# Kernel optimization log

Measured on AMD Instinct MI355X. Metric: run time of the kernel, lower is better.

The kernel has to match this reference:

```python
import jax, jax.numpy as jnp
import numpy as np

B, S, L, D = 32, 8, 128, 768
A, T = 10, 8
VOCAB = 1000


def setup_inputs() -> dict:
    key = jax.random.key(0)
    k1, k2, k3, k4, k5 = jax.random.split(key, 5)
    sentence_ids = jax.random.randint(k1, (B, S, L), 0, VOCAB)
    sentence_attention_masks = jnp.ones((B, S, L), dtype=jnp.float32)
    # precomputed sum of last 4 BERT hidden layers (backbone excluded)
    sentence_embeddings = jax.random.normal(k2, (B, S, L, D), dtype=jnp.float32)
    predicate_ids = jax.random.randint(k3, (B, S, A, T), 0, VOCAB)
    arg0_ids = jax.random.randint(k4, (B, S, A, T), 0, VOCAB)
    arg1_ids = jax.random.randint(k5, (B, S, A, T), 0, VOCAB)
    return {
        "sentence_ids": sentence_ids,
        "sentence_attention_masks": sentence_attention_masks,
        "sentence_embeddings": sentence_embeddings,
        "predicate_ids": predicate_ids,
        "arg0_ids": arg0_ids,
        "arg1_ids": arg1_ids,
    }


def _mean_pool(emb, mask):
    # emb: [b,s,l,d], mask: [b,s,l] -> [b,s,d]
    masked_sum = jnp.einsum('bsld,bsl->bsd', emb, mask)
    counts = jnp.clip(mask.sum(-1, keepdims=True), 1, None)
    return masked_sum / counts


def _arg_embedding(arg_ids, sentence_ids, emb):
    # arg_ids: [b,s,a,t] int, sentence_ids: [b,s,l] int, emb: [b,s,l,d]
    # match[b,s,a,t,l] = sentence token l equals arg token t (and arg token != 0)
    match = (sentence_ids[:, :, None, None, :] == arg_ids[..., None]) & (arg_ids[..., None] != 0)
    mf = match.astype(emb.dtype)
    counts = mf.sum(-1)                                   # [b,s,a,t]
    summed = jnp.einsum('bsatl,bsld->bsatd', mf, emb)      # [b,s,a,t,d]
    avg = summed / jnp.maximum(counts, 1.0)[..., None]
    has = counts > 0                                       # [b,s,a,t]
    t_dim = arg_ids.shape[-1]
    # original loop overwrites per token -> keep the LAST token with a match
    last = (t_dim - 1) - jnp.argmax(has[..., ::-1], axis=-1)  # [b,s,a]
    sel = jnp.take_along_axis(avg, last[..., None, None], axis=3)[:, :, :, 0, :]
    valid = has.any(-1)                                    # [b,s,a]
    return jnp.where(valid[..., None], sel, jnp.zeros((), emb.dtype))


def reference(sentence_ids, sentence_attention_masks, sentence_embeddings,
              predicate_ids, arg0_ids, arg1_ids):
    sentence_embeddings_avg = _mean_pool(sentence_embeddings, sentence_attention_masks)
    predicate_embeddings = _arg_embedding(predicate_ids, sentence_ids, sentence_embeddings)
    arg0_embeddings = _arg_embedding(arg0_ids, sentence_ids, sentence_embeddings)
    arg1_embeddings = _arg_embedding(arg1_ids, sentence_ids, sentence_embeddings)
    return (sentence_embeddings_avg, predicate_embeddings, arg0_embeddings, arg1_embeddings)
```

## Files before the change

### kernel.cpp

```cpp
#include <hip/hip_runtime.h>

#define Bq 32
#define Sq 8
#define Lq 128
#define Dq 768
#define Aq 10
#define Tq 8

typedef float f32x4 __attribute__((ext_vector_type(4)));

constexpr int D4    = Dq / 4;
constexpr int NBS   = Bq * Sq;
constexpr int NBSA  = NBS * Aq;
constexpr int NPOOL = NBS;
constexpr int NARG  = NBS;

__global__ __launch_bounds__(192) void srl_fused_k(
    const int* __restrict__ sids, const float* __restrict__ mask,
    const float* __restrict__ emb, const int* __restrict__ pred,
    const int* __restrict__ a0, const int* __restrict__ a1,
    float* __restrict__ out)
{
    int bid = blockIdx.x;
    int tid = threadIdx.x;

    if (bid < NPOOL) {
        int bs = bid;
        __shared__ float marr[Lq];
        __shared__ float msum;

        if (tid < Lq) marr[tid] = mask[(size_t)bs * Lq + tid];
        if (tid < 64) {
            float mv = mask[(size_t)bs * Lq + tid] +
                       mask[(size_t)bs * Lq + 64 + tid];
            for (int off = 32; off > 0; off >>= 1)
                mv += __shfl_xor(mv, off);
            if (tid == 0) msum = mv;
        }
        __syncthreads();

        const f32x4* eb = (const f32x4*)emb + (size_t)bs * Lq * D4 + tid;
        f32x4 acc = {0.f, 0.f, 0.f, 0.f};
#pragma unroll 16
        for (int l = 0; l < Lq; ++l) {
            float m  = marr[l];
            f32x4 v  = __builtin_nontemporal_load(&eb[(size_t)l * D4]);
            acc += v * m;
        }
        float inv = 1.0f / fmaxf(msum, 1.0f);
        f32x4 r = acc * inv;
        __builtin_nontemporal_store(r, (f32x4*)out + (size_t)bs * D4 + tid);
        return;
    }

    int bs   = bid - NPOOL;
    int set  = tid >> 6;
    int lane = tid & 63;
    const int* ids = (set == 0) ? pred : ((set == 1) ? a0 : a1);

    int s0 = sids[(size_t)bs * Lq + lane];
    int s1 = sids[(size_t)bs * Lq + 64 + lane];

    const f32x4* eb = (const f32x4*)emb + (size_t)bs * Lq * D4;

    for (int a = 0; a < Aq; ++a) {
        int bsa = bs * Aq + a;
        int idv = (lane < Tq) ? ids[(size_t)bsa * Tq + lane] : 0;

        unsigned long long B0 = 0, B1 = 0;
        int ccount = 0;
#pragma unroll
        for (int t = Tq - 1; t >= 0; --t) {
            if (ccount == 0) {
                int idt = __shfl(idv, t);
                if (idt != 0) {
                    unsigned long long b0 = __ballot(s0 == idt);
                    unsigned long long b1 = __ballot(s1 == idt);
                    int c = (int)(__popcll(b0) + __popcll(b1));
                    if (c > 0) { B0 = b0; B1 = b1; ccount = c; }
                }
            }
        }

        f32x4 acc0 = {0.f, 0.f, 0.f, 0.f};
        f32x4 acc1 = acc0, acc2 = acc0;
        unsigned long long b = B0;
        while (b) {
            int l = (int)__builtin_ctzll(b); b &= b - 1;
            acc0 += eb[(size_t)l * D4 + lane];
            acc1 += eb[(size_t)l * D4 + 64 + lane];
            acc2 += eb[(size_t)l * D4 + 128 + lane];
        }
        b = B1;
        while (b) {
            int l = (int)__builtin_ctzll(b) + 64; b &= b - 1;
            acc0 += eb[(size_t)l * D4 + lane];
            acc1 += eb[(size_t)l * D4 + 64 + lane];
            acc2 += eb[(size_t)l * D4 + 128 + lane];
        }

        float inv = (ccount > 0) ? 1.0f / (float)ccount : 0.0f;
        f32x4* o4 = (f32x4*)out +
                    ((size_t)NBS + (size_t)set * NBSA + bsa) * D4;
        __builtin_nontemporal_store(acc0 * inv, o4 + lane);
        __builtin_nontemporal_store(acc1 * inv, o4 + 64 + lane);
        __builtin_nontemporal_store(acc2 * inv, o4 + 128 + lane);
    }
}

extern "C" void kernel_launch(void* const* d_in, const int* in_sizes, int n_in,
                              void* d_out, int out_size, void* d_ws, size_t ws_size,
                              hipStream_t stream) {
    const int*   sids = (const int*)d_in[0];
    const float* mask = (const float*)d_in[1];
    const float* emb  = (const float*)d_in[2];
    const int*   pred = (const int*)d_in[3];
    const int*   a0   = (const int*)d_in[4];
    const int*   a1   = (const int*)d_in[5];
    float* out = (float*)d_out;

    srl_fused_k<<<NPOOL + NARG, 192, 0, stream>>>(sids, mask, emb,
                                                  pred, a0, a1, out);
}
```

Measured before the change: 28.06 us.

## Split work into single-wavefront blocks, three per (b,s) for pool and args

Each pooling block of 192 threads becomes three 64-thread blocks, each covering a third of the D dimension. Each argument block becomes three blocks, one per id set. This triples the number of blocks so more CUs get work and one wave's latency no longer stalls the other two. Non-temporal loads and stores are replaced with ordinary ones, which lets the arg-kernel gathers hit in cache lines the pool blocks already loaded. In exchange the mask is loaded and reduced redundantly in each of the three pool blocks, and there are more small blocks to schedule.

```diff
diff --git a/kernel.cpp b/kernel.cpp
--- a/kernel.cpp
+++ b/kernel.cpp
@@ -12,50 +12,50 @@
 constexpr int D4    = Dq / 4;
 constexpr int NBS   = Bq * Sq;
 constexpr int NBSA  = NBS * Aq;
-constexpr int NPOOL = NBS;
-constexpr int NARG  = NBS;
+constexpr int NPOOL = NBS * 3;
+constexpr int NARG  = NBS * 3;
 
-__global__ __launch_bounds__(192) void srl_fused_k(
+__global__ __launch_bounds__(64) void srl_fused_k(
     const int* __restrict__ sids, const float* __restrict__ mask,
     const float* __restrict__ emb, const int* __restrict__ pred,
     const int* __restrict__ a0, const int* __restrict__ a1,
     float* __restrict__ out)
 {
-    int bid = blockIdx.x;
-    int tid = threadIdx.x;
+    int bid  = blockIdx.x;
+    int lane = threadIdx.x;
 
     if (bid < NPOOL) {
-        int bs = bid;
+        int bs    = bid / 3;
+        int third = bid - bs * 3;
+
         __shared__ float marr[Lq];
-        __shared__ float msum;
-
-        if (tid < Lq) marr[tid] = mask[(size_t)bs * Lq + tid];
-        if (tid < 64) {
-            float mv = mask[(size_t)bs * Lq + tid] +
-                       mask[(size_t)bs * Lq + 64 + tid];
-            for (int off = 32; off > 0; off >>= 1)
-                mv += __shfl_xor(mv, off);
-            if (tid == 0) msum = mv;
-        }
+        float m0 = mask[(size_t)bs * Lq + lane];
+        float m1 = mask[(size_t)bs * Lq + 64 + lane];
+        marr[lane]      = m0;
+        marr[64 + lane] = m1;
+        float mv = m0 + m1;
+        for (int off = 32; off > 0; off >>= 1)
+            mv += __shfl_xor(mv, off);
+        float inv = 1.0f / fmaxf(mv, 1.0f);
         __syncthreads();
 
-        const f32x4* eb = (const f32x4*)emb + (size_t)bs * Lq * D4 + tid;
+        const f32x4* eb = (const f32x4*)emb +
+                          (size_t)bs * Lq * D4 + third * 64 + lane;
         f32x4 acc = {0.f, 0.f, 0.f, 0.f};
 #pragma unroll 16
         for (int l = 0; l < Lq; ++l) {
-            float m  = marr[l];
-            f32x4 v  = __builtin_nontemporal_load(&eb[(size_t)l * D4]);
+            float m = marr[l];
+            f32x4 v = eb[(size_t)l * D4];
             acc += v * m;
         }
-        float inv = 1.0f / fmaxf(msum, 1.0f);
         f32x4 r = acc * inv;
-        __builtin_nontemporal_store(r, (f32x4*)out + (size_t)bs * D4 + tid);
+        ((f32x4*)out)[(size_t)bs * D4 + third * 64 + lane] = r;
         return;
     }
 
-    int bs   = bid - NPOOL;
-    int set  = tid >> 6;
-    int lane = tid & 63;
+    int j   = bid - NPOOL;
+    int bs  = j / 3;
+    int set = j - bs * 3;
     const int* ids = (set == 0) ? pred : ((set == 1) ? a0 : a1);
 
     int s0 = sids[(size_t)bs * Lq + lane];
@@ -102,9 +102,9 @@
         float inv = (ccount > 0) ? 1.0f / (float)ccount : 0.0f;
         f32x4* o4 = (f32x4*)out +
                     ((size_t)NBS + (size_t)set * NBSA + bsa) * D4;
-        __builtin_nontemporal_store(acc0 * inv, o4 + lane);
-        __builtin_nontemporal_store(acc1 * inv, o4 + 64 + lane);
-        __builtin_nontemporal_store(acc2 * inv, o4 + 128 + lane);
+        o4[lane]       = acc0 * inv;
+        o4[64 + lane]  = acc1 * inv;
+        o4[128 + lane] = acc2 * inv;
     }
 }
 
@@ -119,6 +119,6 @@
     const int*   a1   = (const int*)d_in[5];
     float* out = (float*)d_out;
 
-    srl_fused_k<<<NPOOL + NARG, 192, 0, stream>>>(sids, mask, emb,
-                                                  pred, a0, a1, out);
+    srl_fused_k<<<NPOOL + NARG, 64, 0, stream>>>(sids, mask, emb,
+                                                 pred, a0, a1, out);
 }
```

New measurement: 26.78 us. -4.6%, faster.
